# Optimization experiments

Hardware: AMD Instinct MI355X
Metric: run time of the kernel (lower is better)

Reference implementation:

```python
import jax, jax.numpy as jnp
import numpy as np

B, L, DIN, D = 16, 1024, 512, 1024  # batch, l_max, input_dim, d_model
ORDER = 2


def setup_inputs() -> dict:
    key = jax.random.key(0)
    ks = jax.random.split(key, 8)
    n = lambda i, shape, sc: jax.random.normal(ks[i], shape, dtype=jnp.float32) * sc
    return {
        "x": n(0, (B, L, DIN), 1.0),
        # project_in (Linear since input_dim != output_dim)
        "Wp": n(1, (DIN, D), DIN ** -0.5),
        "bp": jnp.zeros((D,), jnp.float32),
        # hyena in_proj -> (order+1)*d channels
        "W_in": n(2, (D, 3 * D), D ** -0.5),
        "b_in": jnp.zeros((3 * D,), jnp.float32),
        # depthwise causal short conv, kernel 3
        "short_w": n(3, (3 * D, 1, 3), 0.5),
        "short_b": jnp.zeros((3 * D,), jnp.float32),
        # implicit long filters (materialized) + per-channel skip bias
        "k_filt": n(4, (ORDER, L, D), 0.02),
        "D_bias": n(5, (ORDER, D), 1.0),
        # hyena out_proj
        "W_out": n(6, (D, D), D ** -0.5),
        "b_out": jnp.zeros((D,), jnp.float32),
    }


def _fftconv(v, k, d_bias):
    # v: [B, L, d], k: [L, d] -> causal long conv via zero-padded FFT + skip
    n = 2 * v.shape[1]
    vf = jnp.fft.rfft(v.astype(jnp.float32), n=n, axis=1)
    kf = jnp.fft.rfft(k.astype(jnp.float32), n=n, axis=0)
    y = jnp.fft.irfft(vf * kf[None], n=n, axis=1)[:, : v.shape[1]]
    return (y + v * d_bias).astype(v.dtype)


def reference(x, Wp, bp, W_in, b_in, short_w, short_b, k_filt, D_bias, W_out, b_out):
    u = x @ Wp + bp                      # [B, L, D] project_in
    u = u @ W_in + b_in                  # [B, L, 3D]
    # depthwise causal short conv over sequence
    uc = jnp.transpose(u, (0, 2, 1))     # [B, 3D, L]
    uc = jax.lax.conv_general_dilated(
        uc, short_w, window_strides=(1,), padding=[(2, 0)],
        feature_group_count=3 * D, dimension_numbers=("NCH", "OIH", "NCH"),
    )[..., :L] + short_b[None, :, None]
    uc = jnp.transpose(uc, (0, 2, 1))    # [B, L, 3D]
    x1, x2, v = jnp.split(uc, 3, axis=-1)
    # Hyena recurrence: gate then long FFT conv, order=2
    v = _fftconv(v * x2, k_filt[0], D_bias[0])
    v = _fftconv(v * x1, k_filt[1], D_bias[1])
    return v @ W_out + b_out             # [B, L, D]
```

## Files before the change

kernel.cpp:

```cpp
#include <hip/hip_runtime.h>

#define BATCH 16
#define LSEQ 1024
#define DIN 512
#define DMODEL 1024
#define D3 3072
#define KCP 1064

typedef __attribute__((ext_vector_type(4))) float f32x4;
typedef __attribute__((ext_vector_type(8))) short bf16x8;

static __device__ __forceinline__ ushort f2bf(float f) {
    uint u = __float_as_uint(f);
    return (ushort)((u + 0x7FFFu + ((u >> 16) & 1u)) >> 16);
}
static __device__ __forceinline__ float bf2f(ushort h) {
    return __uint_as_float(((uint)h) << 16);
}

#define GLD16(ldst, gsrc)                                                        \
    __builtin_amdgcn_global_load_lds(                                            \
        (const __attribute__((address_space(1))) void*)(gsrc),                   \
        (__attribute__((address_space(3))) void*)(ldst), 16, 0, 0)

template <typename OutT, bool HAS_BIAS>
__global__ __launch_bounds__(256) void gemm_mfma(const ushort* __restrict__ A,
                                                 const ushort* __restrict__ Bt,
                                                 const float* __restrict__ bias,
                                                 OutT* __restrict__ C,
                                                 int M, int N, int K) {
    __shared__ ushort Als[2][128 * 32];
    __shared__ ushort Bls[2][128 * 32];
    int nwg = gridDim.x * gridDim.y;
    int bid = blockIdx.y * gridDim.x + blockIdx.x;
    bid = (bid & 7) * (nwg >> 3) + (bid >> 3);
    int n0 = (bid % gridDim.x) * 128, m0 = (bid / gridDim.x) * 128;
    int t = threadIdx.x;
    int w = t >> 6, l = t & 63;
    int wm = w & 1, wn = w >> 1;
    f32x4 acc[4][4] = {};

    int rowA = t >> 2;
    int kb = (t & 3) * 8;
    const ushort* gA0 = A + (size_t)(m0 + rowA) * K + kb;
    const ushort* gA1 = gA0 + (size_t)64 * K;
    const ushort* gB0 = Bt + (size_t)(n0 + rowA) * K + kb;
    const ushort* gB1 = gB0 + (size_t)64 * K;
    int so = 512 * w;

    int aoff = (wm * 64 + (l & 15)) * 32 + (l >> 4) * 8;
    int boff = (wn * 64 + (l & 15)) * 32 + (l >> 4) * 8;

    GLD16(&Als[0][so], gA0);
    GLD16(&Als[0][2048 + so], gA1);
    GLD16(&Bls[0][so], gB0);
    GLD16(&Bls[0][2048 + so], gB1);
    GLD16(&Als[1][so], gA0 + 32);
    GLD16(&Als[1][2048 + so], gA1 + 32);
    GLD16(&Bls[1][so], gB0 + 32);
    GLD16(&Bls[1][2048 + so], gB1 + 32);

    int cur = 0;
    for (int k0 = 0; k0 < K; k0 += 32) {
        if (k0 + 32 < K)
            asm volatile("s_waitcnt vmcnt(4)" ::: "memory");
        else
            asm volatile("s_waitcnt vmcnt(0)" ::: "memory");
        __builtin_amdgcn_s_barrier();
        __builtin_amdgcn_sched_barrier(0);
        bf16x8 af[4], bg[4];
#pragma unroll
        for (int i = 0; i < 4; i++) af[i] = *(const bf16x8*)&Als[cur][aoff + i * 512];
#pragma unroll
        for (int j = 0; j < 4; j++) bg[j] = *(const bf16x8*)&Bls[cur][boff + j * 512];
#pragma unroll
        for (int i = 0; i < 4; i++)
#pragma unroll
            for (int j = 0; j < 4; j++)
                acc[i][j] = __builtin_amdgcn_mfma_f32_16x16x32_bf16(af[i], bg[j],
                                                                    acc[i][j], 0, 0, 0);
        asm volatile("s_waitcnt lgkmcnt(0)" ::: "memory");
        __builtin_amdgcn_sched_barrier(0);
        __builtin_amdgcn_s_barrier();
        if (k0 + 64 < K) {
            GLD16(&Als[cur][so], gA0 + k0 + 64);
            GLD16(&Als[cur][2048 + so], gA1 + k0 + 64);
            GLD16(&Bls[cur][so], gB0 + k0 + 64);
            GLD16(&Bls[cur][2048 + so], gB1 + k0 + 64);
        }
        cur ^= 1;
    }

#pragma unroll
    for (int j = 0; j < 4; j++) {
        int col = n0 + wn * 64 + 16 * j + (l & 15);
        float bv = HAS_BIAS ? bias[col] : 0.f;
#pragma unroll
        for (int i = 0; i < 4; i++) {
            int row0 = m0 + wm * 64 + 16 * i + (l >> 4) * 4;
#pragma unroll
            for (int r = 0; r < 4; r++) {
                float v = acc[i][j][r] + bv;
                if constexpr (sizeof(OutT) == 2)
                    C[(size_t)(row0 + r) * N + col] = (OutT)f2bf(v);
                else
                    C[(size_t)(row0 + r) * N + col] = (OutT)v;
            }
        }
    }
}

__global__ __launch_bounds__(512, 2) void conv_mfma(const ushort* __restrict__ At,
                                                    const ushort* __restrict__ X1t,
                                                    const float* __restrict__ kt,
                                                    const float* __restrict__ Db,
                                                    ushort* __restrict__ V2t, int nb) {
    __shared__ ushort a_lds[16 * 1024];
    __shared__ ushort kc[8 * KCP];
    int d = blockIdx.x;
    int tid = threadIdx.x;
    int w = tid >> 6, l = tid & 63;
    int lr = l & 15, lq = l >> 4;

    {
        int b = tid >> 5, s = tid & 31;
        const ushort* g = At + ((size_t)b * DMODEL + d) * LSEQ + s * 32;
#pragma unroll
        for (int j = 0; j < 4; j++) {
            uint4 v = {0u, 0u, 0u, 0u};
            if (b < nb) v = *(const uint4*)(g + 8 * j);
            int byte = (b * 1024 + s * 32 + 8 * j) * 2;
            *(uint4*)((char*)a_lds + (byte ^ (b << 4))) = v;
        }
    }

    int p = (7 - lr) & 7;
    int v0 = 1023 - lr + 8 * lq - p;
    int a_base = lr * 2048 + lq * 16;
    int swz = lr << 4;
    const int tis[4] = {w, 31 - w, 8 + w, 23 - w};
    int ti0 = tis[0], ti1 = tis[1], ti2 = tis[2], ti3 = tis[3];

    ushort gpre[4][2][4];
#pragma unroll
    for (int ii = 0; ii < 4; ii++)
#pragma unroll
        for (int h = 0; h < 2; h++)
#pragma unroll
            for (int r = 0; r < 4; r++) {
                int b = lq * 4 + r;
                int t2 = 32 * tis[ii] + 16 * h + lr;
                gpre[ii][h][r] = (b < nb)
                    ? X1t[((size_t)b * DMODEL + d) * LSEQ + t2] : (ushort)0;
            }

    for (int o = 0; o < 2; o++) {
        const float* krow = kt + ((size_t)o * DMODEL + d) * LSEQ;
        for (int idx = tid; idx < 8 * KCP; idx += 512) {
            int pp = idx / KCP;
            int u = idx - pp * KCP;
            int ki = 1023 - u - pp;
            kc[idx] = f2bf((ki >= 0) ? krow[ki] : 0.f);
        }
        __syncthreads();

        f32x4 a00 = {}, a01 = {}, a10 = {}, a11 = {};
        f32x4 a20 = {}, a21 = {}, a30 = {}, a31 = {};
        const char* kbp = (const char*)kc + ((size_t)p * KCP + v0) * 2;
        for (int m = 0; m < 32; m++) {
            bf16x8 b0 = *(const bf16x8*)(kbp - 64 * m);
            bf16x8 b1 = *(const bf16x8*)(kbp - 64 * m - 32);
            __builtin_amdgcn_s_setprio(1);
#define CSTEP(TI, A0, A1)                                                      \
            if ((TI) >= m) {                                                   \
                bf16x8 af = *(const bf16x8*)((const char*)a_lds +              \
                                             ((a_base + 64 * ((TI) - m)) ^ swz)); \
                A0 = __builtin_amdgcn_mfma_f32_16x16x32_bf16(af, b0, A0, 0, 0, 0); \
                A1 = __builtin_amdgcn_mfma_f32_16x16x32_bf16(af, b1, A1, 0, 0, 0); \
            }
            CSTEP(ti0, a00, a01)
            CSTEP(ti1, a10, a11)
            CSTEP(ti2, a20, a21)
            CSTEP(ti3, a30, a31)
#undef CSTEP
            __builtin_amdgcn_s_setprio(0);
        }
        float db = Db[o * DMODEL + d];
        __syncthreads();
#define CEPI(II, TI, AC, H)                                                    \
        {                                                                      \
            _Pragma("unroll")                                                  \
            for (int r = 0; r < 4; r++) {                                      \
                int t2 = 32 * (TI) + 16 * (H) + lr;                            \
                int b = lq * 4 + r;                                            \
                int ab = ((b * 1024 + t2) * 2) ^ (b << 4);                     \
                float a0v = bf2f(*(const ushort*)((const char*)a_lds + ab));   \
                float y = (AC)[r] + a0v * db;                                  \
                if (o == 0) y *= bf2f(gpre[II][H][r]);                         \
                *(ushort*)((char*)a_lds + ab) = f2bf(y);                       \
            }                                                                  \
        }
        CEPI(0, ti0, a00, 0) CEPI(0, ti0, a01, 1)
        CEPI(1, ti1, a10, 0) CEPI(1, ti1, a11, 1)
        CEPI(2, ti2, a20, 0) CEPI(2, ti2, a21, 1)
        CEPI(3, ti3, a30, 0) CEPI(3, ti3, a31, 1)
#undef CEPI
    }
    __syncthreads();
    {
        int b = tid >> 5, s = tid & 31;
        if (b < nb) {
            ushort* g = V2t + ((size_t)b * DMODEL + d) * LSEQ + s * 32;
#pragma unroll
            for (int j = 0; j < 4; j++) {
                int byte = (b * 1024 + s * 32 + 8 * j) * 2;
                uint4 v = *(const uint4*)((const char*)a_lds + (byte ^ (b << 4)));
                *(uint4*)(g + 8 * j) = v;
            }
        }
    }
}

__global__ void cvt_bf16(const float* __restrict__ in, ushort* __restrict__ out, int n4) {
    int i = blockIdx.x * blockDim.x + threadIdx.x;
    if (i >= n4) return;
    float4 v = *(const float4*)&in[4 * i];
    uint2 pk;
    pk.x = (uint)f2bf(v.x) | ((uint)f2bf(v.y) << 16);
    pk.y = (uint)f2bf(v.z) | ((uint)f2bf(v.w) << 16);
    *(uint2*)&out[4 * i] = pk;
}

__global__ void transpose_cvt(const float* __restrict__ in, ushort* __restrict__ out,
                              int R, int C) {
    __shared__ float tile[32][33];
    int c0 = blockIdx.x * 32, r0 = blockIdx.y * 32;
    int tx = threadIdx.x, ty = threadIdx.y;
#pragma unroll
    for (int i = 0; i < 4; i++)
        tile[ty + 8 * i][tx] = in[(size_t)(r0 + ty + 8 * i) * C + c0 + tx];
    __syncthreads();
#pragma unroll
    for (int i = 0; i < 4; i++)
        out[(size_t)(c0 + ty + 8 * i) * R + r0 + tx] = f2bf(tile[tx][ty + 8 * i]);
}

__global__ __launch_bounds__(256) void transpose_b16(const ushort* __restrict__ in,
                                                     ushort* __restrict__ out) {
    __shared__ uint tile[64][33];
    int t0 = blockIdx.x * 64, d0 = blockIdx.y * 64, b = blockIdx.z;
    int i = threadIdx.x;
    const ushort* ip = in + (size_t)b * DMODEL * LSEQ;
    ushort* op = out + (size_t)b * LSEQ * DMODEL;
    int dl = i >> 5, cu = i & 31;
#pragma unroll
    for (int j = 0; j < 8; j++)
        tile[dl + 8 * j][cu] =
            *(const uint*)&ip[(size_t)(d0 + dl + 8 * j) * LSEQ + t0 + 2 * cu];
    __syncthreads();
    int du = i & 31, tb = i >> 5;
#pragma unroll
    for (int j = 0; j < 8; j++) {
        int tl = tb + 8 * j;
        uint lo = (tile[2 * du][tl >> 1] >> (16 * (tl & 1))) & 0xFFFFu;
        uint hi = (tile[2 * du + 1][tl >> 1] >> (16 * (tl & 1))) & 0xFFFFu;
        *(uint*)&op[(size_t)(t0 + tl) * DMODEL + d0 + 2 * du] = lo | (hi << 16);
    }
}

__global__ void bias_fuse(const float* __restrict__ bp, const float* __restrict__ W_in,
                          const float* __restrict__ b_in, float* __restrict__ bf) {
    int n = blockIdx.x * blockDim.x + threadIdx.x;
    float s = b_in[n];
    for (int k = 0; k < DMODEL; k++) s += bp[k] * W_in[(size_t)k * D3 + n];
    bf[n] = s;
}

__global__ void transpose_k(const float* __restrict__ kf, float* __restrict__ kt) {
    __shared__ float tile[32][33];
    int s0 = blockIdx.x * 32, d0 = blockIdx.y * 32, o = blockIdx.z;
    int tx = threadIdx.x, ty = threadIdx.y;
#pragma unroll
    for (int i = 0; i < 4; i++)
        tile[ty + 8 * i][tx] = kf[((size_t)o * LSEQ + s0 + ty + 8 * i) * DMODEL + d0 + tx];
    __syncthreads();
#pragma unroll
    for (int i = 0; i < 4; i++)
        kt[((size_t)o * DMODEL + d0 + ty + 8 * i) * LSEQ + s0 + tx] = tile[tx][ty + 8 * i];
}

__global__ __launch_bounds__(256) void shortconv_gate(const ushort* __restrict__ UC,
                                                      const float* __restrict__ sw,
                                                      const float* __restrict__ sb,
                                                      ushort* __restrict__ At,
                                                      ushort* __restrict__ X1t) {
    __shared__ uint tin[34][33];
    __shared__ ushort oA[64][34];
    __shared__ ushort oX[64][34];
    int t0 = blockIdx.x * 32, c0 = blockIdx.y * 64, b = blockIdx.z;
    int tx = threadIdx.x, ty = threadIdx.y;
    float2 res[3][4];
#pragma unroll
    for (int g = 0; g < 3; g++) {
        int ch = g * DMODEL + c0 + 2 * tx;
        __syncthreads();
        for (int r = ty; r < 34; r += 8) {
            int t = t0 + r - 2;
            tin[r][tx] = (t >= 0)
                ? *(const uint*)&UC[((size_t)b * LSEQ + t) * D3 + ch] : 0u;
        }
        __syncthreads();
        float w00 = sw[ch * 3 + 0], w01 = sw[ch * 3 + 1], w02 = sw[ch * 3 + 2];
        float w10 = sw[ch * 3 + 3], w11 = sw[ch * 3 + 4], w12 = sw[ch * 3 + 5];
        float bb0 = sb[ch], bb1 = sb[ch + 1];
#pragma unroll
        for (int i = 0; i < 4; i++) {
            int r = ty + 8 * i + 2;
            uint u0 = tin[r - 2][tx], u1 = tin[r - 1][tx], u2 = tin[r][tx];
            res[g][i].x = w00 * bf2f((ushort)u0) + w01 * bf2f((ushort)u1) +
                          w02 * bf2f((ushort)u2) + bb0;
            res[g][i].y = w10 * bf2f((ushort)(u0 >> 16)) + w11 * bf2f((ushort)(u1 >> 16)) +
                          w12 * bf2f((ushort)(u2 >> 16)) + bb1;
        }
    }
#pragma unroll
    for (int i = 0; i < 4; i++) {
        int t = ty + 8 * i;
        oA[2 * tx][t]     = f2bf(res[2][i].x * res[1][i].x);
        oA[2 * tx + 1][t] = f2bf(res[2][i].y * res[1][i].y);
        oX[2 * tx][t]     = f2bf(res[0][i].x);
        oX[2 * tx + 1][t] = f2bf(res[0][i].y);
    }
    __syncthreads();
    int li = ty * 32 + tx;
    int row = li >> 2, cu0 = (li & 3) * 4;
    ushort* gA = At  + ((size_t)b * DMODEL + c0 + row) * LSEQ + t0;
    ushort* gX = X1t + ((size_t)b * DMODEL + c0 + row) * LSEQ + t0;
#pragma unroll
    for (int j = 0; j < 4; j++) {
        int cu = cu0 + j;
        uint av = (uint)oA[row][2 * cu] | ((uint)oA[row][2 * cu + 1] << 16);
        uint xv = (uint)oX[row][2 * cu] | ((uint)oX[row][2 * cu + 1] << 16);
        *(uint*)&gA[2 * cu] = av;
        *(uint*)&gX[2 * cu] = xv;
    }
}

extern "C" void kernel_launch(void* const* d_in, const int* in_sizes, int n_in,
                              void* d_out, int out_size, void* d_ws, size_t ws_size,
                              hipStream_t stream) {
    (void)in_sizes; (void)n_in; (void)out_size;
    const float* x    = (const float*)d_in[0];
    const float* Wp   = (const float*)d_in[1];
    const float* bp   = (const float*)d_in[2];
    const float* W_in = (const float*)d_in[3];
    const float* b_in = (const float*)d_in[4];
    const float* sw   = (const float*)d_in[5];
    const float* sb   = (const float*)d_in[6];
    const float* kf   = (const float*)d_in[7];
    const float* Db   = (const float*)d_in[8];
    const float* Wout = (const float*)d_in[9];
    const float* bout = (const float*)d_in[10];
    float* out = (float*)d_out;

    char* ws = (char*)d_ws;
    ushort* Wf_t   = (ushort*)(ws);
    float*  bfv    = (float*)(ws + 3145728);
    float*  kt     = (float*)(ws + 3162112);
    ushort* Wout_t = (ushort*)(ws + 11550720);
    const size_t PB = 13647872;

    const size_t XB  = 1048576;
    const size_t ATB = 2097152;
    const size_t X1B = 2097152;
    const size_t UCB = 6291456;
    const size_t V2B = 2097152;
    const size_t PREPB = 7340032;

    int cb = 1, cf = 1;
    {
        bool ok = false;
        for (int tcb = 16; tcb >= 1 && !ok; tcb >>= 1) {
            for (int tcf = tcb; tcf >= 1; tcf >>= 1) {
                size_t ucreg = (size_t)tcf * UCB;
                size_t v2need = (size_t)2 * tcb * V2B;
                if (ucreg < v2need) ucreg = v2need;
                if (ucreg < PREPB) ucreg = PREPB;
                size_t need = PB + (size_t)tcb * (XB + ATB + X1B) + ucreg;
                if (need <= ws_size) { cb = tcb; cf = tcf; ok = true; break; }
            }
        }
    }

    ushort* x_bf = (ushort*)(ws + PB);
    ushort* Atb  = (ushort*)(ws + PB + (size_t)cb * XB);
    ushort* X1tb = (ushort*)(ws + PB + (size_t)cb * (XB + ATB));
    char*   ucrg = ws + PB + (size_t)cb * (XB + ATB + X1B);
    ushort* UC   = (ushort*)ucrg;
    ushort* V2t  = (ushort*)ucrg;
    ushort* V2   = (ushort*)(ucrg + (size_t)cb * V2B);
    ushort* W_inT = (ushort*)ucrg;
    ushort* Wp_bf = (ushort*)(ucrg + 6291456);

    transpose_cvt<<<dim3(96, 32), dim3(32, 8), 0, stream>>>(W_in, W_inT, DMODEL, D3);
    cvt_bf16<<<512, 256, 0, stream>>>(Wp, Wp_bf, DIN * DMODEL / 4);
    gemm_mfma<ushort, false><<<dim3(4, 24), 256, 0, stream>>>(W_inT, Wp_bf, nullptr,
                                                              Wf_t, D3, DIN, DMODEL);
    bias_fuse<<<D3 / 256, 256, 0, stream>>>(bp, W_in, b_in, bfv);
    transpose_cvt<<<dim3(32, 32), dim3(32, 8), 0, stream>>>(Wout, Wout_t, DMODEL, DMODEL);
    transpose_k<<<dim3(32, 32, 2), dim3(32, 8), 0, stream>>>(kf, kt);

    for (int b0 = 0; b0 < BATCH; b0 += cb) {
        cvt_bf16<<<cb * LSEQ * DIN / 1024, 256, 0, stream>>>(
            x + (size_t)b0 * LSEQ * DIN, x_bf, cb * LSEQ * DIN / 4);
        for (int f0 = 0; f0 < cb; f0 += cf) {
            gemm_mfma<ushort, true><<<dim3(24, cf * 8), 256, 0, stream>>>(
                x_bf + (size_t)f0 * LSEQ * DIN, Wf_t, bfv, UC, cf * LSEQ, D3, DIN);
            shortconv_gate<<<dim3(32, 16, cf), dim3(32, 8), 0, stream>>>(
                UC, sw, sb, Atb + (size_t)f0 * DMODEL * LSEQ,
                X1tb + (size_t)f0 * DMODEL * LSEQ);
        }
        conv_mfma<<<DMODEL, 512, 0, stream>>>(Atb, X1tb, kt, Db, V2t, cb);
        transpose_b16<<<dim3(16, 16, cb), dim3(256), 0, stream>>>(V2t, V2);
        gemm_mfma<float, true><<<dim3(8, cb * 8), 256, 0, stream>>>(
            V2, Wout_t, bout, out + (size_t)b0 * LSEQ * DMODEL, cb * LSEQ, DMODEL, DMODEL);
    }
}
```

Measured before the change: 414.3 us.

## Pair adjacent output tiles per wave to reuse LDS A-fragments across MFMAs

Reassigns each wave's four output time-tiles to two adjacent pairs (2w, 2w+1) and (30-2w, 31-2w). The A fragment loaded for the lower tile at step m is held in registers and reused for the following tile at step m+1, which halves LDS fragment reads in the Toeplitz-MFMA inner loop. The gate prefetch of X1t into registers is removed and the gate is read from global memory in the epilogue. That frees registers but puts a global load latency into the epilogue.

Measured after the change: 415.7 us. No clear change (+0.3%).

```diff
diff --git a/kernel.cpp b/kernel.cpp
--- a/kernel.cpp
+++ b/kernel.cpp
@@ -138,21 +138,11 @@
     int v0 = 1023 - lr + 8 * lq - p;
     int a_base = lr * 2048 + lq * 16;
     int swz = lr << 4;
-    const int tis[4] = {w, 31 - w, 8 + w, 23 - w};
-    int ti0 = tis[0], ti1 = tis[1], ti2 = tis[2], ti3 = tis[3];
-
-    ushort gpre[4][2][4];
-#pragma unroll
-    for (int ii = 0; ii < 4; ii++)
-#pragma unroll
-        for (int h = 0; h < 2; h++)
-#pragma unroll
-            for (int r = 0; r < 4; r++) {
-                int b = lq * 4 + r;
-                int t2 = 32 * tis[ii] + 16 * h + lr;
-                gpre[ii][h][r] = (b < nb)
-                    ? X1t[((size_t)b * DMODEL + d) * LSEQ + t2] : (ushort)0;
-            }
+    int tL0 = 2 * w, tF0 = 2 * w + 1;
+    int tL1 = 30 - 2 * w, tF1 = 31 - 2 * w;
+
+#define AFB(BLK) (*(const bf16x8*)((const char*)a_lds + ((a_base + 64 * (BLK)) ^ swz)))
+#define MF(AF, B, AC) AC = __builtin_amdgcn_mfma_f32_16x16x32_bf16(AF, B, AC, 0, 0, 0)
 
     for (int o = 0; o < 2; o++) {
         const float* krow = kt + ((size_t)o * DMODEL + d) * LSEQ;
@@ -164,30 +154,43 @@
         }
         __syncthreads();
 
-        f32x4 a00 = {}, a01 = {}, a10 = {}, a11 = {};
-        f32x4 a20 = {}, a21 = {}, a30 = {}, a31 = {};
+        f32x4 aL0l = {}, aL0h = {}, aF0l = {}, aF0h = {};
+        f32x4 aL1l = {}, aL1h = {}, aF1l = {}, aF1h = {};
         const char* kbp = (const char*)kc + ((size_t)p * KCP + v0) * 2;
-        for (int m = 0; m < 32; m++) {
+        bf16x8 hold0, hold1;
+        {
+            bf16x8 b0 = *(const bf16x8*)(kbp);
+            bf16x8 b1 = *(const bf16x8*)(kbp - 32);
+            __builtin_amdgcn_s_setprio(1);
+            bf16x8 f0 = AFB(tF0);
+            MF(f0, b0, aF0l); MF(f0, b1, aF0h);
+            hold0 = AFB(tL0);
+            MF(hold0, b0, aL0l); MF(hold0, b1, aL0h);
+            bf16x8 f1 = AFB(tF1);
+            MF(f1, b0, aF1l); MF(f1, b1, aF1h);
+            hold1 = AFB(tL1);
+            MF(hold1, b0, aL1l); MF(hold1, b1, aL1h);
+            __builtin_amdgcn_s_setprio(0);
+        }
+        for (int m = 1; m < 32; m++) {
             bf16x8 b0 = *(const bf16x8*)(kbp - 64 * m);
             bf16x8 b1 = *(const bf16x8*)(kbp - 64 * m - 32);
             __builtin_amdgcn_s_setprio(1);
-#define CSTEP(TI, A0, A1)                                                      \
-            if ((TI) >= m) {                                                   \
-                bf16x8 af = *(const bf16x8*)((const char*)a_lds +              \
-                                             ((a_base + 64 * ((TI) - m)) ^ swz)); \
-                A0 = __builtin_amdgcn_mfma_f32_16x16x32_bf16(af, b0, A0, 0, 0, 0); \
-                A1 = __builtin_amdgcn_mfma_f32_16x16x32_bf16(af, b1, A1, 0, 0, 0); \
+            if (m <= tF0) { MF(hold0, b0, aF0l); MF(hold0, b1, aF0h); }
+            if (m <= tL0) {
+                hold0 = AFB(tL0 - m);
+                MF(hold0, b0, aL0l); MF(hold0, b1, aL0h);
             }
-            CSTEP(ti0, a00, a01)
-            CSTEP(ti1, a10, a11)
-            CSTEP(ti2, a20, a21)
-            CSTEP(ti3, a30, a31)
-#undef CSTEP
+            if (m <= tF1) { MF(hold1, b0, aF1l); MF(hold1, b1, aF1h); }
+            if (m <= tL1) {
+                hold1 = AFB(tL1 - m);
+                MF(hold1, b0, aL1l); MF(hold1, b1, aL1h);
+            }
             __builtin_amdgcn_s_setprio(0);
         }
         float db = Db[o * DMODEL + d];
         __syncthreads();
-#define CEPI(II, TI, AC, H)                                                    \
+#define CEPI(TI, AC, H)                                                        \
         {                                                                      \
             _Pragma("unroll")                                                  \
             for (int r = 0; r < 4; r++) {                                      \
@@ -196,16 +199,22 @@
                 int ab = ((b * 1024 + t2) * 2) ^ (b << 4);                     \
                 float a0v = bf2f(*(const ushort*)((const char*)a_lds + ab));   \
                 float y = (AC)[r] + a0v * db;                                  \
-                if (o == 0) y *= bf2f(gpre[II][H][r]);                         \
+                if (o == 0) {                                                  \
+                    float g = (b < nb)                                         \
+                        ? bf2f(X1t[((size_t)b * DMODEL + d) * LSEQ + t2]) : 0.f; \
+                    y *= g;                                                    \
+                }                                                              \
                 *(ushort*)((char*)a_lds + ab) = f2bf(y);                       \
             }                                                                  \
         }
-        CEPI(0, ti0, a00, 0) CEPI(0, ti0, a01, 1)
-        CEPI(1, ti1, a10, 0) CEPI(1, ti1, a11, 1)
-        CEPI(2, ti2, a20, 0) CEPI(2, ti2, a21, 1)
-        CEPI(3, ti3, a30, 0) CEPI(3, ti3, a31, 1)
+        CEPI(tL0, aL0l, 0) CEPI(tL0, aL0h, 1)
+        CEPI(tF0, aF0l, 0) CEPI(tF0, aF0h, 1)
+        CEPI(tL1, aL1l, 0) CEPI(tL1, aL1h, 1)
+        CEPI(tF1, aF1l, 0) CEPI(tF1, aF1h, 1)
 #undef CEPI
     }
+#undef AFB
+#undef MF
     __syncthreads();
     {
         int b = tid >> 5, s = tid & 31;
```
